# Optimization experiments

Hardware: AMD Instinct MI355X
Metric: run time of the kernel (lower is better)

## Reference

```python
import jax, jax.numpy as jnp
import numpy as np

B, S, T, E, H, VIN, VOUT = 64, 64, 32, 512, 1024, 32000, 32000


def setup_inputs() -> dict:
    key = jax.random.key(0)
    ks = jax.random.split(key, 12)
    rn = lambda k, shape, s=0.02: jax.random.normal(k, shape, jnp.float32) * s
    return {
        "src": jax.random.randint(ks[0], (B, S), 0, VIN),
        "tgt": jax.random.randint(ks[1], (B, T), 0, VOUT),
        "enc_emb": rn(ks[2], (VIN, E)),
        "dec_emb": rn(ks[3], (VOUT, E)),
        "enc_Wih": rn(ks[4], (4 * H, E)),
        "enc_Whh": rn(ks[5], (4 * H, H)),
        "enc_bih": jnp.zeros((4 * H,), jnp.float32),
        "enc_bhh": jnp.zeros((4 * H,), jnp.float32),
        "dec_Wih": rn(ks[6], (4 * H, E + H)),
        "dec_Whh": rn(ks[7], (4 * H, H)),
        "dec_bih": jnp.zeros((4 * H,), jnp.float32),
        "dec_bhh": jnp.zeros((4 * H,), jnp.float32),
        "attn_W": rn(ks[8], (H, 2 * H)),
        "attn_b": jnp.zeros((H,), jnp.float32),
        "v": jax.random.uniform(ks[9], (H,), jnp.float32),
        "fc_W": rn(ks[10], (VOUT, 2 * H)),
        "fc_b": jnp.zeros((VOUT,), jnp.float32),
    }


def _lstm_cell(x, h, c, Wih, Whh, bih, bhh):
    # torch gate order: i, f, g, o
    gates = x @ Wih.T + bih + h @ Whh.T + bhh
    i, f, g, o = jnp.split(gates, 4, axis=-1)
    c_new = jax.nn.sigmoid(f) * c + jax.nn.sigmoid(i) * jnp.tanh(g)
    h_new = jax.nn.sigmoid(o) * jnp.tanh(c_new)
    return h_new, c_new


def _forward(src, tgt, enc_emb, dec_emb, enc_Wih, enc_Whh, enc_bih, enc_bhh,
             dec_Wih, dec_Whh, dec_bih, dec_bhh, attn_W, attn_b, v, fc_W, fc_b):
    b, s = src.shape
    t_len = tgt.shape[1]
    hdim = enc_Whh.shape[1]

    # ---- encoder (single-layer LSTM, batch_first) ----
    x = enc_emb[src]  # [B,S,E] (dropout=0 in eval)

    def enc_step(carry, x_t):
        h, c = carry
        h, c = _lstm_cell(x_t, h, c, enc_Wih, enc_Whh, enc_bih, enc_bhh)
        return (h, c), h

    h0 = jnp.zeros((b, hdim), x.dtype)
    (h_f, c_f), enc_out_tm = jax.lax.scan(enc_step, (h0, h0), jnp.swapaxes(x, 0, 1))
    enc_out = jnp.swapaxes(enc_out_tm, 0, 1)  # [B,S,H]

    # hidden.detach() in torch
    h_f = jax.lax.stop_gradient(h_f)
    c_f = jax.lax.stop_gradient(c_f)

    # split attn_W for the concat(hidden, enc_out) linear
    Wh, We = attn_W[:, :hdim], attn_W[:, hdim:]
    enc_proj = jnp.einsum('bsh,kh->bsk', enc_out, We)  # hoisted, [B,S,H]

    def dec_step(carry, tok):
        h, c = carry
        emb = dec_emb[tok]  # [B,E]
        # Bahdanau attention: tanh(Linear(cat(h, enc_out))) . v
        energy = jnp.tanh(h @ Wh.T[None] if False else jnp.tanh((h @ Wh.T)[:, None, :] + enc_proj + attn_b))
        energy = jnp.tanh((h @ Wh.T)[:, None, :] + enc_proj + attn_b)  # [B,S,H]
        scores = jnp.einsum('bsh,h->bs', energy, v)
        a = jax.nn.softmax(scores, axis=1)
        context = jnp.einsum('bs,bsh->bh', a, enc_out)  # [B,H]
        rnn_in = jnp.concatenate([emb, context], axis=-1)
        h_new, c_new = _lstm_cell(rnn_in, h, c, dec_Wih, dec_Whh, dec_bih, dec_bhh)
        logits = jnp.concatenate([h_new, context], axis=-1) @ fc_W.T + fc_b
        return (h_new, c_new), logits

    # teacher_forcing_ratio = 1.0 -> input at step t is tgt[:, t-1]
    toks_tm = jnp.swapaxes(tgt[:, : t_len - 1], 0, 1)  # [T-1, B]
    _, logits_tm = jax.lax.scan(dec_step, (h_f, c_f), toks_tm)  # [T-1,B,V]
    logits = jnp.swapaxes(logits_tm, 0, 1)  # [B,T-1,V]
    zeros0 = jnp.zeros((b, 1, fc_W.shape[0]), logits.dtype)
    return jnp.concatenate([zeros0, logits], axis=1)  # [B,T,V]


def reference(src, tgt, enc_emb, dec_emb, enc_Wih, enc_Whh, enc_bih, enc_bhh,
              dec_Wih, dec_Whh, dec_bih, dec_bhh, attn_W, attn_b, v, fc_W, fc_b):
    return _forward(src, tgt, enc_emb, dec_emb, enc_Wih, enc_Whh, enc_bih, enc_bhh,
                    dec_Wih, dec_Whh, dec_bih, dec_bhh, attn_W, attn_b, v, fc_W, fc_b)
```

## Files before the change

### kernel.cpp

```cpp
#include <hip/hip_runtime.h>
#include <hip/hip_bf16.h>

typedef __bf16 bf16x8 __attribute__((ext_vector_type(8)));
typedef float  f32x4  __attribute__((ext_vector_type(4)));
typedef _Float16 h16x8 __attribute__((ext_vector_type(8)));

__device__ __forceinline__ unsigned short f2b(float f) {
    union { float f; unsigned u; } w; w.f = f;
    unsigned u = w.u + 0x7FFF + ((w.u >> 16) & 1);
    return (unsigned short)(u >> 16);
}
__device__ __forceinline__ float tanhfast(float x) {
    float e = __expf(2.0f * x);
    return 1.0f - 2.0f / (e + 1.0f);
}

__device__ __forceinline__ void stU(unsigned* p, unsigned v) {
    __hip_atomic_store(p, v, __ATOMIC_RELAXED, __HIP_MEMORY_SCOPE_AGENT);
}
__device__ __forceinline__ void stF(float* p, float v) {
    __hip_atomic_store(p, v, __ATOMIC_RELAXED, __HIP_MEMORY_SCOPE_AGENT);
}
__device__ __forceinline__ int ldI(const int* p) {
    return __hip_atomic_load((int*)p, __ATOMIC_RELAXED, __HIP_MEMORY_SCOPE_AGENT);
}
__device__ __forceinline__ void stI(int* p, int v) {
    __hip_atomic_store(p, v, __ATOMIC_RELAXED, __HIP_MEMORY_SCOPE_AGENT);
}

#define GLD16(g, l) __builtin_amdgcn_global_load_lds( \
    (const __attribute__((address_space(1))) void*)(g), \
    (__attribute__((address_space(3))) void*)(l), 16, 0, 0)

#define SLOT_STRIDE 16
#define NPOLL 256

__device__ __forceinline__ void gbar(int* slots, int* gen, int target) {
    asm volatile("s_waitcnt vmcnt(0)" ::: "memory");
    __syncthreads();
    if (blockIdx.x == 0) {
        if (threadIdx.x == 0) stI(slots, target);
        if (threadIdx.x < NPOLL) {
            while (ldI(slots + threadIdx.x * SLOT_STRIDE) < target)
                __builtin_amdgcn_s_sleep(1);
        }
        __syncthreads();
        if (threadIdx.x == 0) stI(gen, target);
    } else {
        if (threadIdx.x == 0) {
            stI(slots + blockIdx.x * SLOT_STRIDE, target);
            while (ldI(gen) < target)
                __builtin_amdgcn_s_sleep(1);
        }
        __syncthreads();
    }
}

__device__ __forceinline__ void mac8(const unsigned short* A, const unsigned short* B,
                                     f32x4& acc) {
    bf16x8 a[8], b[8];
#pragma unroll
    for (int kk = 0; kk < 8; ++kk) {
        a[kk] = *(const bf16x8*)(A + kk * 32);
        b[kk] = *(const bf16x8*)(B + kk * 32);
    }
#pragma unroll
    for (int kk = 0; kk < 8; ++kk)
        acc = __builtin_amdgcn_mfma_f32_16x16x32_bf16(a[kk], b[kk], acc, 0, 0, 0);
}
__device__ __forceinline__ void mac4(const unsigned short* A, const unsigned short* B,
                                     f32x4& acc) {
    bf16x8 a[4], b[4];
#pragma unroll
    for (int kk = 0; kk < 4; ++kk) {
        a[kk] = *(const bf16x8*)(A + kk * 32);
        b[kk] = *(const bf16x8*)(B + kk * 32);
    }
#pragma unroll
    for (int kk = 0; kk < 4; ++kk)
        acc = __builtin_amdgcn_mfma_f32_16x16x32_bf16(a[kk], b[kk], acc, 0, 0, 0);
}


__global__ void k_gather(const float* __restrict__ emb, const int* __restrict__ tok,
                         unsigned short* __restrict__ out, int L, int ldtok) {
    long total = (long)L * 64 * 128;
    for (long i = (long)blockIdx.x * blockDim.x + threadIdx.x; i < total;
         i += (long)gridDim.x * blockDim.x) {
        int  e4 = (int)(i & 127);
        long r  = i >> 7;
        int  t  = (int)(r >> 6), b = (int)(r & 63);
        int  tk = tok[b * ldtok + t];
        float4 v = *(const float4*)(emb + (long)tk * 512 + e4 * 4);
        ushort4 o; o.x = f2b(v.x); o.y = f2b(v.y); o.z = f2b(v.z); o.w = f2b(v.w);
        *(ushort4*)(out + r * 512 + e4 * 4) = o;
    }
}

__global__ void k_conv(const float* __restrict__ in, unsigned short* __restrict__ out,
                       long N_, int K_, int ldin, int col0, int ldout, int outcol0, int reorder) {
    long total = N_ * (K_ >> 2);
    int kq = K_ >> 2;
    for (long i = (long)blockIdx.x * blockDim.x + threadIdx.x; i < total;
         i += (long)gridDim.x * blockDim.x) {
        long n = i / kq;
        int  k4 = (int)(i - n * kq) * 4;
        long row = reorder ? (long)((n & 3) * 1024 + (n >> 2)) : n;
        float4 v = *(const float4*)(in + row * ldin + col0 + k4);
        ushort4 o; o.x = f2b(v.x); o.y = f2b(v.y); o.z = f2b(v.z); o.w = f2b(v.w);
        *(ushort4*)(out + n * ldout + outcol0 + k4) = o;
    }
}

__global__ void k_bias(const float* __restrict__ b1, const float* __restrict__ b2,
                       float* __restrict__ out) {
    int n = blockIdx.x * blockDim.x + threadIdx.x;
    if (n < 4096) {
        int row = (n & 3) * 1024 + (n >> 2);
        out[n] = b1[row] + b2[row];
    }
}

__global__ void k_zero0(float* __restrict__ out) {
    long total = 64L * 8000;
    for (long i = (long)blockIdx.x * blockDim.x + threadIdx.x; i < total;
         i += (long)gridDim.x * blockDim.x) {
        int b = (int)(i / 8000), q = (int)(i % 8000);
        float4 z = {0.f, 0.f, 0.f, 0.f};
        *(float4*)(out + (long)b * 1024000 + q * 4) = z;
    }
}

template<int BM, int BN, int WGM, int WGN, int FM, int FN>
__device__ __forceinline__ void gemm_core(
    const unsigned short* __restrict__ A, int lda,
    const unsigned short* __restrict__ B, int ldb,
    long m0, long n0, int K,
    unsigned short* As, unsigned short* Bs,
    f32x4 (&acc)[FM][FN])
{
    const int tid  = threadIdx.x;
    const int lane = tid & 63;
    const int wave = tid >> 6;
    const int wm = wave / WGN;
    const int wn = wave % WGN;
    const int srow = lane >> 2;
    const int scol = (lane & 3) * 8;
    const int frow = lane & 15;
    const int fcol = (lane >> 4) * 8;

    for (int k0 = 0; k0 < K; k0 += 32) {
        __syncthreads();
        for (int c = wave; c < BM / 16; c += 4) {
            const unsigned short* g = A + (m0 + c * 16 + srow) * (long)lda + k0 + scol;
            GLD16(g, As + c * 512);
        }
        for (int c = wave; c < BN / 16; c += 4) {
            const unsigned short* g = B + (n0 + c * 16 + srow) * (long)ldb + k0 + scol;
            GLD16(g, Bs + c * 512);
        }
        __syncthreads();
        bf16x8 af[FM], bfr[FN];
#pragma unroll
        for (int m = 0; m < FM; ++m)
            af[m] = *(const bf16x8*)(As + ((wm * FM + m) * 16 + frow) * 32 + fcol);
#pragma unroll
        for (int n = 0; n < FN; ++n)
            bfr[n] = *(const bf16x8*)(Bs + ((wn * FN + n) * 16 + frow) * 32 + fcol);
#pragma unroll
        for (int m = 0; m < FM; ++m)
#pragma unroll
            for (int n = 0; n < FN; ++n)
                acc[m][n] = __builtin_amdgcn_mfma_f32_16x16x32_bf16(af[m], bfr[n], acc[m][n], 0, 0, 0);
    }
}

template<int BM, int BN, int WGM, int WGN, int FM, int FN, int MODE>
__global__ __launch_bounds__(256) void k_gemm(
    const unsigned short* __restrict__ A, int lda,
    const unsigned short* __restrict__ B, int ldb,
    float* __restrict__ C, long ldc, const float* __restrict__ bias,
    int M, int N, int K, int Mreal)
{
    __shared__ __align__(16) unsigned short As[BM * 32];
    __shared__ __align__(16) unsigned short Bs[BN * 32];
    long m0, n0;
    if (MODE == 1) {
        int bid = blockIdx.x;
        int n = (bid & 7) * 32 + (bid >> 7);
        int m = (bid >> 3) & 15;
        if (n >= 250) return;
        m0 = (long)m * BM; n0 = (long)n * BN;
    } else {
        m0 = (long)blockIdx.y * BM; n0 = (long)blockIdx.x * BN;
    }
    f32x4 acc[FM][FN] = {};
    gemm_core<BM, BN, WGM, WGN, FM, FN>(A, lda, B, ldb, m0, n0, K, As, Bs, acc);

    const int lane = threadIdx.x & 63;
    const int wave = threadIdx.x >> 6;
    const int wm = wave / WGN, wn = wave % WGN;
#pragma unroll
    for (int n = 0; n < FN; ++n) {
        long col = n0 + wn * FN * 16 + n * 16 + (lane & 15);
        float bv = bias ? bias[col] : 0.0f;
#pragma unroll
        for (int m = 0; m < FM; ++m) {
            int rl = wm * FM * 16 + m * 16 + (lane >> 4) * 4;
#pragma unroll
            for (int q = 0; q < 4; ++q) {
                long r = m0 + rl + q;
                float val = acc[m][n][q] + bv;
                if (MODE == 0) {
                    C[r * ldc + col] = val;
                } else if (MODE == 2) {
                    ((_Float16*)C)[r * ldc + col] = (_Float16)val;
                } else {
                    if (r < Mreal) {
                        long orow = (r & 63) * 32 + (r >> 6) + 1;
                        C[orow * ldc + col] = val;
                    }
                }
            }
        }
    }
}

__global__ __launch_bounds__(512, 2) void k_enc(
    const unsigned short* __restrict__ W,
    const float* __restrict__ pre,
    unsigned short* __restrict__ hsl,
    unsigned short* __restrict__ enc_out,
    unsigned short* __restrict__ eoT,
    unsigned short* __restrict__ hS0,
    float* __restrict__ cspill,
    int* slots, int* gen)
{
    __shared__ float gs[64 * 16];
    const int blk = blockIdx.x, tid = threadIdx.x;
    const int lane = tid & 63, wave = tid >> 6;
    const int rt = wave >> 1, kh = wave & 1;
    const int n0 = blk * 16;
    const int arow = rt * 16 + (lane & 15);
    const int kch = kh * 512 + (lane >> 4) * 8;
    const int grow = (rt * 16 + (lane >> 4) * 4) * 16 + (lane & 15);
    const unsigned short* Bw = W + (long)(n0 + (lane & 15)) * 1024 + kch;
    const int pb = tid >> 1, pjl = (tid & 1) * 2;
    const int jg = blk * 4 + pjl;
    float c0 = 0.f, c1 = 0.f;
    float4 pr0 = {}, pr1 = {};
    if (tid < 128) {
        pr0 = *(const float4*)(pre + (long)pb * 4096 + n0 + pjl * 4);
        pr1 = *(const float4*)(pre + (long)pb * 4096 + n0 + pjl * 4 + 4);
    }
    int bt = 0;
    for (int t = 0; t < 64; ++t) {
        const unsigned short* Ar = hsl + (long)t * 65536 + (long)arow * 1024 + kch;
        f32x4 acc = {};
        mac8(Ar, Bw, acc);
        mac8(Ar + 256, Bw + 256, acc);
        if (kh == 0) {
#pragma unroll
            for (int q = 0; q < 4; ++q) gs[grow + q * 16] = acc[q];
        }
        __syncthreads();
        if (kh == 1) {
#pragma unroll
            for (int q = 0; q < 4; ++q) atomicAdd(&gs[grow + q * 16], acc[q]);
        }
        __syncthreads();
        if (tid < 128) {
            float4 gA = *(const float4*)(gs + pb * 16 + pjl * 4);
            float4 gB = *(const float4*)(gs + pb * 16 + pjl * 4 + 4);
            float h0v, h1v;
            {
                float gi = gA.x + pr0.x, gf = gA.y + pr0.y, gg = gA.z + pr0.z, go = gA.w + pr0.w;
                float i_ = 1.f / (1.f + __expf(-gi)), f_ = 1.f / (1.f + __expf(-gf));
                float g_ = tanhfast(gg), o_ = 1.f / (1.f + __expf(-go));
                c0 = f_ * c0 + i_ * g_; h0v = o_ * tanhfast(c0);
            }
            {
                float gi = gB.x + pr1.x, gf = gB.y + pr1.y, gg = gB.z + pr1.z, go = gB.w + pr1.w;
                float i_ = 1.f / (1.f + __expf(-gi)), f_ = 1.f / (1.f + __expf(-gf));
                float g_ = tanhfast(gg), o_ = 1.f / (1.f + __expf(-go));
                c1 = f_ * c1 + i_ * g_; h1v = o_ * tanhfast(c1);
            }
            unsigned short hb0 = f2b(h0v), hb1 = f2b(h1v);
            unsigned pk = (unsigned)hb0 | ((unsigned)hb1 << 16);
            stU((unsigned*)(hsl + (long)(t + 1) * 65536 + (long)pb * 1024 + jg), pk);
            *(unsigned*)(enc_out + ((long)pb * 64 + t) * 1024 + jg) = pk;
            eoT[((long)pb * 1024 + jg) * 64 + t]     = hb0;
            eoT[((long)pb * 1024 + jg + 1) * 64 + t] = hb1;
            if (t < 63) {
                pr0 = *(const float4*)(pre + (long)(t + 1) * 262144 + (long)pb * 4096 + n0 + pjl * 4);
                pr1 = *(const float4*)(pre + (long)(t + 1) * 262144 + (long)pb * 4096 + n0 + pjl * 4 + 4);
            } else {
                *(unsigned*)(hS0 + (long)pb * 1024 + jg) = pk;
                cspill[(long)pb * 1024 + jg]     = c0;
                cspill[(long)pb * 1024 + jg + 1] = c1;
            }
        }
        gbar(slots, gen, ++bt);
    }
}

__global__ __launch_bounds__(512, 2) void k_dec(
    const unsigned short* __restrict__ Wh,
    const unsigned short* __restrict__ Wc,
    const float* __restrict__ pre,
    const _Float16* __restrict__ proj16,
    const unsigned short* __restrict__ eoT,
    const float* __restrict__ v,
    const float* __restrict__ cspill,
    unsigned short* __restrict__ hS,
    unsigned short* __restrict__ ctxS,
    float* __restrict__ qS,
    unsigned short* __restrict__ fcin,
    int* slots, int* gen)
{
    __shared__ float gs[64 * 16];
    __shared__ float qv[1024], vv[1024];
    __shared__ float sc[64], al[64];
    const int blk = blockIdx.x, tid = threadIdx.x;
    const int lane = tid & 63, wave = tid >> 6;
    const int rt = wave >> 1, kh = wave & 1;
    const int n0 = blk * 16;
    const int grow = (rt * 16 + (lane >> 4) * 4) * 16 + (lane & 15);
    const int pb = tid >> 1, pjl = (tid & 1) * 2;
    const int jg = blk * 4 + pjl;
    if (tid < 256) {
        float4 v4 = *(const float4*)(v + tid * 4);
        *(float4*)(vv + tid * 4) = v4;
    }
    float c0 = 0.f, c1 = 0.f;
    if (tid < 128) {
        c0 = cspill[(long)pb * 1024 + jg];
        c1 = cspill[(long)pb * 1024 + jg + 1];
    }
    __syncthreads();
    int bt = 0;
    for (int t = 0; t < 31; ++t) {
        const unsigned short* hSt   = hS   + (long)t * 65536;
        const unsigned short* ctxSt = ctxS + (long)t * 65536;
        float4 pr0 = {}, pr1 = {};
        if (tid < 128) {
            pr0 = *(const float4*)(pre + (long)t * 262144 + (long)pb * 4096 + n0 + pjl * 4);
            pr1 = *(const float4*)(pre + (long)t * 262144 + (long)pb * 4096 + n0 + pjl * 4 + 4);
        }
        {
            int nq = blk >> 2, mt = blk & 3;
            if (tid < 256) gs[tid] = 0.f;
            __syncthreads();
            const unsigned short* Ar = hSt + (long)(mt * 16 + (lane & 15)) * 1024
                                           + wave * 128 + (lane >> 4) * 8;
            const unsigned short* Bq = Wh + (long)(nq * 16 + (lane & 15)) * 1024
                                          + wave * 128 + (lane >> 4) * 8;
            f32x4 qa = {};
            mac4(Ar, Bq, qa);
#pragma unroll
            for (int q = 0; q < 4; ++q)
                atomicAdd(&gs[((lane >> 4) * 4 + q) * 16 + (lane & 15)], qa[q]);
            __syncthreads();
            if (tid < 256)
                stF(qS + (long)t * 65536 + (long)(mt * 16 + (tid >> 4)) * 1024
                        + nq * 16 + (tid & 15), gs[tid]);
        }
        gbar(slots, gen, ++bt);
        if (blk < 64) {
            const int b = blk;
            if (tid < 256)
                *(float4*)(qv + tid * 4) =
                    *(const float4*)(qS + (long)t * 65536 + (long)b * 1024 + tid * 4);
            __syncthreads();
            int s = tid >> 3, part = tid & 7;
            const h16x8* pp = (const h16x8*)(proj16 + ((long)b * 64 + s) * 1024 + part * 128);
            float a_ = 0.f;
#pragma unroll 4
            for (int d = 0; d < 16; ++d) {
                h16x8 pv = pp[d];
                int h = part * 128 + d * 8;
#pragma unroll
                for (int j = 0; j < 8; ++j)
                    a_ += vv[h + j] * tanhfast(qv[h + j] + (float)pv[j]);
            }
            a_ += __shfl_xor(a_, 1);
            a_ += __shfl_xor(a_, 2);
            a_ += __shfl_xor(a_, 4);
            if (part == 0) sc[s] = a_;
            __syncthreads();
            if (tid < 64) {
                float x = sc[tid], mx = x;
                for (int o = 32; o; o >>= 1) mx = fmaxf(mx, __shfl_xor(mx, o));
                float e = __expf(x - mx), su = e;
                for (int o = 32; o; o >>= 1) su += __shfl_xor(su, o);
                al[tid] = e / su;
            }
            __syncthreads();
            int h0 = tid * 2;
            float cacc[2];
#pragma unroll
            for (int r = 0; r < 2; ++r) {
                const bf16x8* ep = (const bf16x8*)(eoT + ((long)b * 1024 + h0 + r) * 64);
                float s_ = 0.f;
#pragma unroll
                for (int c8 = 0; c8 < 8; ++c8) {
                    bf16x8 v8 = ep[c8];
#pragma unroll
                    for (int jj = 0; jj < 8; ++jj)
                        s_ += al[c8 * 8 + jj] * (float)v8[jj];
                }
                cacc[r] = s_;
            }
            unsigned pk0 = (unsigned)f2b(cacc[0]) | ((unsigned)f2b(cacc[1]) << 16);
            stU((unsigned*)(ctxS + (long)t * 65536 + (long)b * 1024 + h0), pk0);
            *(unsigned*)(fcin + ((long)t * 64 + b) * 2048 + 1024 + h0) = pk0;
        }
        gbar(slots, gen, ++bt);
        {
            const unsigned short* Asrc = (kh ? ctxSt : hSt)
                + (long)(rt * 16 + (lane & 15)) * 1024 + (lane >> 4) * 8;
            const unsigned short* Bw = Wc + (long)(n0 + (lane & 15)) * 2048
                                          + kh * 1024 + (lane >> 4) * 8;
            f32x4 acc = {};
            mac8(Asrc,       Bw,       acc);
            mac8(Asrc + 256, Bw + 256, acc);
            mac8(Asrc + 512, Bw + 512, acc);
            mac8(Asrc + 768, Bw + 768, acc);
            if (kh == 0) {
#pragma unroll
                for (int q = 0; q < 4; ++q) gs[grow + q * 16] = acc[q];
            }
            __syncthreads();
            if (kh == 1) {
#pragma unroll
                for (int q = 0; q < 4; ++q) atomicAdd(&gs[grow + q * 16], acc[q]);
            }
            __syncthreads();
            if (tid < 128) {
                float4 gA = *(const float4*)(gs + pb * 16 + pjl * 4);
                float4 gB = *(const float4*)(gs + pb * 16 + pjl * 4 + 4);
                float h0v, h1v;
                {
                    float gi = gA.x + pr0.x, gf = gA.y + pr0.y, gg = gA.z + pr0.z, go = gA.w + pr0.w;
                    float i_ = 1.f / (1.f + __expf(-gi)), f_ = 1.f / (1.f + __expf(-gf));
                    float g_ = tanhfast(gg), o_ = 1.f / (1.f + __expf(-go));
                    c0 = f_ * c0 + i_ * g_; h0v = o_ * tanhfast(c0);
                }
                {
                    float gi = gB.x + pr1.x, gf = gB.y + pr1.y, gg = gB.z + pr1.z, go = gB.w + pr1.w;
                    float i_ = 1.f / (1.f + __expf(-gi)), f_ = 1.f / (1.f + __expf(-gf));
                    float g_ = tanhfast(gg), o_ = 1.f / (1.f + __expf(-go));
                    c1 = f_ * c1 + i_ * g_; h1v = o_ * tanhfast(c1);
                }
                unsigned pk = (unsigned)f2b(h0v) | ((unsigned)f2b(h1v) << 16);
                stU((unsigned*)(hS + (long)(t + 1) * 65536 + (long)pb * 1024 + jg), pk);
                *(unsigned*)(fcin + ((long)t * 64 + pb) * 2048 + jg) = pk;
            }
        }
        gbar(slots, gen, ++bt);
    }
}

extern "C" void kernel_launch(void* const* d_in, const int* in_sizes, int n_in,
                              void* d_out, int out_size, void* d_ws, size_t ws_size,
                              hipStream_t stream) {
    const int*   src     = (const int*)d_in[0];
    const int*   tgt     = (const int*)d_in[1];
    const float* enc_emb = (const float*)d_in[2];
    const float* dec_emb = (const float*)d_in[3];
    const float* enc_Wih = (const float*)d_in[4];
    const float* enc_Whh = (const float*)d_in[5];
    const float* enc_bih = (const float*)d_in[6];
    const float* enc_bhh = (const float*)d_in[7];
    const float* dec_Wih = (const float*)d_in[8];
    const float* dec_Whh = (const float*)d_in[9];
    const float* dec_bih = (const float*)d_in[10];
    const float* dec_bhh = (const float*)d_in[11];
    const float* attn_W  = (const float*)d_in[12];
    const float* attn_b  = (const float*)d_in[13];
    const float* vvec    = (const float*)d_in[14];
    const float* fc_W    = (const float*)d_in[15];
    const float* fc_b    = (const float*)d_in[16];
    float* out = (float*)d_out;

    char* ws = (char*)d_ws;
    size_t off = 0;
    auto alloc = [&](size_t bytes) -> char* {
        off = (off + 255) & ~(size_t)255;
        char* p = ws + off; off += bytes; return p;
    };
    unsigned short* wX      = (unsigned short*)alloc(4096UL * 512 * 2);
    unsigned short* weWih   = (unsigned short*)alloc(4096UL * 512 * 2);
    unsigned short* weWhh   = (unsigned short*)alloc(4096UL * 1024 * 2);
    float*          ebias   = (float*)alloc(4096UL * 4);
    float*          pre_enc = (float*)alloc(4096UL * 4096 * 4);
    unsigned short* enc_out = (unsigned short*)alloc(4096UL * 1024 * 2);
    unsigned short* eoT     = (unsigned short*)alloc(64UL * 1024 * 64 * 2);
    unsigned short* wWe     = (unsigned short*)alloc(1024UL * 1024 * 2);
    unsigned short* wWh     = (unsigned short*)alloc(1024UL * 1024 * 2);
    _Float16*       proj16  = (_Float16*)alloc(4096UL * 1024 * 2);
    float*          cbuf    = (float*)alloc(64UL * 1024 * 4);
    unsigned short* demb    = (unsigned short*)alloc(2048UL * 512 * 2);
    unsigned short* wDemb   = (unsigned short*)alloc(4096UL * 512 * 2);
    unsigned short* wCat    = (unsigned short*)alloc(4096UL * 2048 * 2);
    float*          dbias   = (float*)alloc(4096UL * 4);
    float*          pre_dec = (float*)alloc(2048UL * 4096 * 4);
    unsigned short* fcin    = (unsigned short*)alloc(2048UL * 2048 * 2);
    unsigned short* wFc     = (unsigned short*)alloc(32000UL * 2048 * 2);
    unsigned short* hslE    = (unsigned short*)alloc(65UL * 65536 * 2);
    unsigned short* hS      = (unsigned short*)alloc(32UL * 65536 * 2);
    unsigned short* ctxS    = (unsigned short*)alloc(32UL * 65536 * 2);
    float*          qS      = (float*)alloc(32UL * 65536 * 4);
    int*            bar     = (int*)alloc(65536);
    (void)ws_size; (void)in_sizes; (void)n_in; (void)out_size;

    int* slotsE = bar;
    int* genE   = bar + 4096;
    int* slotsD = bar + 8192;
    int* genD   = bar + 12288;

    hipMemsetAsync(bar, 0, 65536, stream);
    hipMemsetAsync(hslE, 0, 65536UL * 2, stream);
    k_zero0<<<512, 256, 0, stream>>>(out);

    k_gather<<<2048, 256, 0, stream>>>(enc_emb, src, wX, 64, 64);
    k_gather<<<1024, 256, 0, stream>>>(dec_emb, tgt, demb, 31, 32);
    k_conv<<<2048, 256, 0, stream>>>(enc_Wih, weWih, 4096, 512, 512, 0, 512, 0, 1);
    k_conv<<<2048, 256, 0, stream>>>(enc_Whh, weWhh, 4096, 1024, 1024, 0, 1024, 0, 1);
    k_conv<<<2048, 256, 0, stream>>>(dec_Wih, wDemb, 4096, 512, 1536, 0, 512, 0, 1);
    k_conv<<<2048, 256, 0, stream>>>(dec_Whh, wCat, 4096, 1024, 1024, 0, 2048, 0, 1);
    k_conv<<<2048, 256, 0, stream>>>(dec_Wih, wCat, 4096, 1024, 1536, 512, 2048, 1024, 1);
    k_conv<<<2048, 256, 0, stream>>>(attn_W, wWh, 1024, 1024, 2048, 0, 1024, 0, 0);
    k_conv<<<2048, 256, 0, stream>>>(attn_W, wWe, 1024, 1024, 2048, 1024, 1024, 0, 0);
    k_conv<<<4096, 256, 0, stream>>>(fc_W, wFc, 32000, 2048, 2048, 0, 2048, 0, 0);
    k_bias<<<16, 256, 0, stream>>>(enc_bih, enc_bhh, ebias);
    k_bias<<<16, 256, 0, stream>>>(dec_bih, dec_bhh, dbias);

    k_gemm<128,128,2,2,4,4,0><<<dim3(32, 32), 256, 0, stream>>>(
        wX, 512, weWih, 512, pre_enc, 4096, ebias, 4096, 4096, 512, 4096);
    k_gemm<128,128,2,2,4,4,0><<<dim3(32, 16), 256, 0, stream>>>(
        demb, 512, wDemb, 512, pre_dec, 4096, dbias, 2048, 4096, 512, 2048);

    k_enc<<<256, 512, 0, stream>>>(weWhh, pre_enc, hslE, enc_out, eoT,
                                   hS, cbuf, slotsE, genE);

    k_gemm<128,128,2,2,4,4,2><<<dim3(8, 32), 256, 0, stream>>>(
        enc_out, 1024, wWe, 1024, (float*)proj16, 1024, attn_b, 4096, 1024, 1024, 4096);

    k_dec<<<256, 512, 0, stream>>>(wWh, wCat, pre_dec, proj16, eoT, vvec, cbuf,
                                   hS, ctxS, qS, fcin, slotsD, genD);

    k_gemm<128,128,2,2,4,4,1><<<dim3(4096), 256, 0, stream>>>(
        fcin, 2048, wFc, 2048, out, 32000, fc_b, 2048, 32000, 2048, 1984);
}
```

Before: 2.595 ms.

## Keep recurrent weights resident in LDS with 128 persistent 1024-thread blocks

The persistent encoder and decoder kernels now run 128 blocks of 1024 threads instead of 256 blocks of 512, and each block owns 32 gate columns. At kernel start each block loads its slice of the recurrent weight matrix into LDS (64 KB for the encoder, 128 KB for the decoder), so every time step reads the MFMA B operands from LDS instead of global memory. The decoder also splits the hidden and context halves of its gate GEMM so the hidden half runs before the attention barrier, overlapping it with the query projection. This lowers per-step global traffic and barrier participants, at the cost of half as many blocks, large LDS use, more shared atomics, and 16-bit atomic stores for h.

New measurement: 3.121 ms. 20.3% more time.

```diff
diff --git a/kernel.cpp b/kernel.cpp
--- a/kernel.cpp
+++ b/kernel.cpp
@@ -18,6 +18,9 @@
 __device__ __forceinline__ void stU(unsigned* p, unsigned v) {
     __hip_atomic_store(p, v, __ATOMIC_RELAXED, __HIP_MEMORY_SCOPE_AGENT);
 }
+__device__ __forceinline__ void stS(unsigned short* p, unsigned short v) {
+    __hip_atomic_store(p, v, __ATOMIC_RELAXED, __HIP_MEMORY_SCOPE_AGENT);
+}
 __device__ __forceinline__ void stF(float* p, float v) {
     __hip_atomic_store(p, v, __ATOMIC_RELAXED, __HIP_MEMORY_SCOPE_AGENT);
 }
@@ -33,14 +36,13 @@
     (__attribute__((address_space(3))) void*)(l), 16, 0, 0)
 
 #define SLOT_STRIDE 16
-#define NPOLL 256
-
-__device__ __forceinline__ void gbar(int* slots, int* gen, int target) {
+
+__device__ __forceinline__ void gbar(int* slots, int* gen, int target, int nblk) {
     asm volatile("s_waitcnt vmcnt(0)" ::: "memory");
     __syncthreads();
     if (blockIdx.x == 0) {
         if (threadIdx.x == 0) stI(slots, target);
-        if (threadIdx.x < NPOLL) {
+        if ((int)threadIdx.x < nblk) {
             while (ldI(slots + threadIdx.x * SLOT_STRIDE) < target)
                 __builtin_amdgcn_s_sleep(1);
         }
@@ -56,17 +58,15 @@
     }
 }
 
-__device__ __forceinline__ void mac8(const unsigned short* A, const unsigned short* B,
-                                     f32x4& acc) {
-    bf16x8 a[8], b[8];
-#pragma unroll
-    for (int kk = 0; kk < 8; ++kk) {
-        a[kk] = *(const bf16x8*)(A + kk * 32);
-        b[kk] = *(const bf16x8*)(B + kk * 32);
-    }
+template<int STR>
+__device__ __forceinline__ void mac8L(const unsigned short* A, const bf16x8* BL,
+                                      f32x4& acc) {
+    bf16x8 a[8];
+#pragma unroll
+    for (int kk = 0; kk < 8; ++kk) a[kk] = *(const bf16x8*)(A + kk * 32);
 #pragma unroll
     for (int kk = 0; kk < 8; ++kk)
-        acc = __builtin_amdgcn_mfma_f32_16x16x32_bf16(a[kk], b[kk], acc, 0, 0, 0);
+        acc = __builtin_amdgcn_mfma_f32_16x16x32_bf16(a[kk], BL[kk * STR], acc, 0, 0, 0);
 }
 __device__ __forceinline__ void mac4(const unsigned short* A, const unsigned short* B,
                                      f32x4& acc) {
@@ -226,7 +226,7 @@
     }
 }
 
-__global__ __launch_bounds__(512, 2) void k_enc(
+__global__ __launch_bounds__(1024, 1) void k_enc(
     const unsigned short* __restrict__ W,
     const float* __restrict__ pre,
     unsigned short* __restrict__ hsl,
@@ -236,75 +236,59 @@
     float* __restrict__ cspill,
     int* slots, int* gen)
 {
-    __shared__ float gs[64 * 16];
+    __shared__ __align__(16) unsigned short WL[32 * 1024];
+    __shared__ float gs[64 * 32];
     const int blk = blockIdx.x, tid = threadIdx.x;
     const int lane = tid & 63, wave = tid >> 6;
-    const int rt = wave >> 1, kh = wave & 1;
-    const int n0 = blk * 16;
-    const int arow = rt * 16 + (lane & 15);
-    const int kch = kh * 512 + (lane >> 4) * 8;
-    const int grow = (rt * 16 + (lane >> 4) * 4) * 16 + (lane & 15);
-    const unsigned short* Bw = W + (long)(n0 + (lane & 15)) * 1024 + kch;
-    const int pb = tid >> 1, pjl = (tid & 1) * 2;
-    const int jg = blk * 4 + pjl;
-    float c0 = 0.f, c1 = 0.f;
-    float4 pr0 = {}, pr1 = {};
-    if (tid < 128) {
-        pr0 = *(const float4*)(pre + (long)pb * 4096 + n0 + pjl * 4);
-        pr1 = *(const float4*)(pre + (long)pb * 4096 + n0 + pjl * 4 + 4);
-    }
+    const int cg = wave >> 3, rt = (wave >> 1) & 3, kh = wave & 1;
+    const int n0 = blk * 32;
+    const int pb = tid >> 3, pj = tid & 7;
+    const int jg = blk * 8 + pj;
+    for (int i = tid; i < 4096; i += 1024) {
+        int r = i & 31, k8 = i >> 5;
+        ((bf16x8*)WL)[k8 * 32 + r] = *(const bf16x8*)(W + (long)(n0 + r) * 1024 + k8 * 8);
+    }
+    const bf16x8* BL = (const bf16x8*)WL + ((long)(kh * 64 + (lane >> 4))) * 32 + cg * 16 + (lane & 15);
+    const int arowoff = (rt * 16 + (lane & 15)) * 1024 + kh * 512 + (lane >> 4) * 8;
+    const int grow = (rt * 16 + (lane >> 4) * 4) * 32 + cg * 16 + (lane & 15);
+    float c0 = 0.f;
+    float4 pr = {};
+    if (tid < 512) pr = *(const float4*)(pre + (long)pb * 4096 + n0 + pj * 4);
+    __syncthreads();
     int bt = 0;
     for (int t = 0; t < 64; ++t) {
-        const unsigned short* Ar = hsl + (long)t * 65536 + (long)arow * 1024 + kch;
+        gs[tid] = 0.f; gs[tid + 1024] = 0.f;
+        __syncthreads();
+        const unsigned short* Ar = hsl + (long)t * 65536 + arowoff;
         f32x4 acc = {};
-        mac8(Ar, Bw, acc);
-        mac8(Ar + 256, Bw + 256, acc);
-        if (kh == 0) {
-#pragma unroll
-            for (int q = 0; q < 4; ++q) gs[grow + q * 16] = acc[q];
-        }
+        mac8L<128>(Ar,       BL,        acc);
+        mac8L<128>(Ar + 256, BL + 1024, acc);
+#pragma unroll
+        for (int q = 0; q < 4; ++q) atomicAdd(&gs[grow + q * 32], acc[q]);
         __syncthreads();
-        if (kh == 1) {
-#pragma unroll
-            for (int q = 0; q < 4; ++q) atomicAdd(&gs[grow + q * 16], acc[q]);
-        }
-        __syncthreads();
-        if (tid < 128) {
-            float4 gA = *(const float4*)(gs + pb * 16 + pjl * 4);
-            float4 gB = *(const float4*)(gs + pb * 16 + pjl * 4 + 4);
-            float h0v, h1v;
-            {
-                float gi = gA.x + pr0.x, gf = gA.y + pr0.y, gg = gA.z + pr0.z, go = gA.w + pr0.w;
-                float i_ = 1.f / (1.f + __expf(-gi)), f_ = 1.f / (1.f + __expf(-gf));
-                float g_ = tanhfast(gg), o_ = 1.f / (1.f + __expf(-go));
-                c0 = f_ * c0 + i_ * g_; h0v = o_ * tanhfast(c0);
-            }
-            {
-                float gi = gB.x + pr1.x, gf = gB.y + pr1.y, gg = gB.z + pr1.z, go = gB.w + pr1.w;
-                float i_ = 1.f / (1.f + __expf(-gi)), f_ = 1.f / (1.f + __expf(-gf));
-                float g_ = tanhfast(gg), o_ = 1.f / (1.f + __expf(-go));
-                c1 = f_ * c1 + i_ * g_; h1v = o_ * tanhfast(c1);
-            }
-            unsigned short hb0 = f2b(h0v), hb1 = f2b(h1v);
-            unsigned pk = (unsigned)hb0 | ((unsigned)hb1 << 16);
-            stU((unsigned*)(hsl + (long)(t + 1) * 65536 + (long)pb * 1024 + jg), pk);
-            *(unsigned*)(enc_out + ((long)pb * 64 + t) * 1024 + jg) = pk;
-            eoT[((long)pb * 1024 + jg) * 64 + t]     = hb0;
-            eoT[((long)pb * 1024 + jg + 1) * 64 + t] = hb1;
+        if (tid < 512) {
+            float4 g4 = *(const float4*)(gs + pb * 32 + pj * 4);
+            float gi = g4.x + pr.x, gf = g4.y + pr.y, gg = g4.z + pr.z, go = g4.w + pr.w;
+            float i_ = 1.f / (1.f + __expf(-gi)), f_ = 1.f / (1.f + __expf(-gf));
+            float g_ = tanhfast(gg), o_ = 1.f / (1.f + __expf(-go));
+            c0 = f_ * c0 + i_ * g_;
+            float hv = o_ * tanhfast(c0);
+            unsigned short hb = f2b(hv);
+            stS(hsl + (long)(t + 1) * 65536 + (long)pb * 1024 + jg, hb);
+            enc_out[((long)pb * 64 + t) * 1024 + jg] = hb;
+            eoT[((long)pb * 1024 + jg) * 64 + t] = hb;
             if (t < 63) {
-                pr0 = *(const float4*)(pre + (long)(t + 1) * 262144 + (long)pb * 4096 + n0 + pjl * 4);
-                pr1 = *(const float4*)(pre + (long)(t + 1) * 262144 + (long)pb * 4096 + n0 + pjl * 4 + 4);
+                pr = *(const float4*)(pre + (long)(t + 1) * 262144 + (long)pb * 4096 + n0 + pj * 4);
             } else {
-                *(unsigned*)(hS0 + (long)pb * 1024 + jg) = pk;
-                cspill[(long)pb * 1024 + jg]     = c0;
-                cspill[(long)pb * 1024 + jg + 1] = c1;
-            }
-        }
-        gbar(slots, gen, ++bt);
-    }
-}
-
-__global__ __launch_bounds__(512, 2) void k_dec(
+                stS(hS0 + (long)pb * 1024 + jg, hb);
+                cspill[(long)pb * 1024 + jg] = c0;
+            }
+        }
+        gbar(slots, gen, ++bt, 128);
+    }
+}
+
+__global__ __launch_bounds__(1024, 1) void k_dec(
     const unsigned short* __restrict__ Wh,
     const unsigned short* __restrict__ Wc,
     const float* __restrict__ pre,
@@ -318,67 +302,78 @@
     unsigned short* __restrict__ fcin,
     int* slots, int* gen)
 {
-    __shared__ float gs[64 * 16];
+    __shared__ __align__(16) unsigned short WcL[32 * 2048];
+    __shared__ float gs1[32 * 16];
+    __shared__ float gs2[64 * 32];
     __shared__ float qv[1024], vv[1024];
     __shared__ float sc[64], al[64];
     const int blk = blockIdx.x, tid = threadIdx.x;
     const int lane = tid & 63, wave = tid >> 6;
-    const int rt = wave >> 1, kh = wave & 1;
-    const int n0 = blk * 16;
-    const int grow = (rt * 16 + (lane >> 4) * 4) * 16 + (lane & 15);
-    const int pb = tid >> 1, pjl = (tid & 1) * 2;
-    const int jg = blk * 4 + pjl;
-    if (tid < 256) {
-        float4 v4 = *(const float4*)(v + tid * 4);
-        *(float4*)(vv + tid * 4) = v4;
-    }
-    float c0 = 0.f, c1 = 0.f;
-    if (tid < 128) {
-        c0 = cspill[(long)pb * 1024 + jg];
-        c1 = cspill[(long)pb * 1024 + jg + 1];
-    }
+    const int n0 = blk * 32;
+    const int cg = wave >> 3, rt = (wave >> 1) & 3, kh = wave & 1;
+    const int rs = wave >> 3, kq = wave & 7;
+    const int nq = blk >> 1, mt = blk & 1;
+    const int pb = tid >> 3, pj = tid & 7;
+    const int jg = blk * 8 + pj;
+    for (int i = tid; i < 8192; i += 1024) {
+        int r = i & 31, k8 = i >> 5;
+        ((bf16x8*)WcL)[k8 * 32 + r] = *(const bf16x8*)(Wc + (long)(n0 + r) * 2048 + k8 * 8);
+    }
+    const bf16x8* BLh = (const bf16x8*)WcL + ((long)(kh * 64 + (lane >> 4))) * 32 + cg * 16 + (lane & 15);
+    const bf16x8* BLc = BLh + 128L * 32;
+    const int garow = (rt * 16 + (lane & 15)) * 1024 + kh * 512 + (lane >> 4) * 8;
+    const int grow = (rt * 16 + (lane >> 4) * 4) * 32 + cg * 16 + (lane & 15);
+    vv[tid] = v[tid];
+    float c0 = 0.f;
+    if (tid < 512) c0 = cspill[(long)pb * 1024 + jg];
     __syncthreads();
     int bt = 0;
     for (int t = 0; t < 31; ++t) {
         const unsigned short* hSt   = hS   + (long)t * 65536;
         const unsigned short* ctxSt = ctxS + (long)t * 65536;
-        float4 pr0 = {}, pr1 = {};
-        if (tid < 128) {
-            pr0 = *(const float4*)(pre + (long)t * 262144 + (long)pb * 4096 + n0 + pjl * 4);
-            pr1 = *(const float4*)(pre + (long)t * 262144 + (long)pb * 4096 + n0 + pjl * 4 + 4);
-        }
+        float4 pr = {};
+        if (tid < 512)
+            pr = *(const float4*)(pre + (long)t * 262144 + (long)pb * 4096 + n0 + pj * 4);
         {
-            int nq = blk >> 2, mt = blk & 3;
-            if (tid < 256) gs[tid] = 0.f;
+            if (tid < 512) gs1[tid] = 0.f;
+            gs2[tid] = 0.f; gs2[tid + 1024] = 0.f;
             __syncthreads();
-            const unsigned short* Ar = hSt + (long)(mt * 16 + (lane & 15)) * 1024
-                                           + wave * 128 + (lane >> 4) * 8;
-            const unsigned short* Bq = Wh + (long)(nq * 16 + (lane & 15)) * 1024
-                                          + wave * 128 + (lane >> 4) * 8;
-            f32x4 qa = {};
-            mac4(Ar, Bq, qa);
-#pragma unroll
-            for (int q = 0; q < 4; ++q)
-                atomicAdd(&gs[((lane >> 4) * 4 + q) * 16 + (lane & 15)], qa[q]);
+            {
+                const unsigned short* Ar = hSt + (long)(mt * 32 + rs * 16 + (lane & 15)) * 1024
+                                               + kq * 128 + (lane >> 4) * 8;
+                const unsigned short* Bq = Wh + (long)(nq * 16 + (lane & 15)) * 1024
+                                              + kq * 128 + (lane >> 4) * 8;
+                f32x4 qa = {};
+                mac4(Ar, Bq, qa);
+#pragma unroll
+                for (int q = 0; q < 4; ++q)
+                    atomicAdd(&gs1[(rs * 16 + (lane >> 4) * 4 + q) * 16 + (lane & 15)], qa[q]);
+            }
+            {
+                const unsigned short* Ah = hSt + garow;
+                f32x4 acc = {};
+                mac8L<128>(Ah,       BLh,        acc);
+                mac8L<128>(Ah + 256, BLh + 1024, acc);
+#pragma unroll
+                for (int q = 0; q < 4; ++q) atomicAdd(&gs2[grow + q * 32], acc[q]);
+            }
             __syncthreads();
-            if (tid < 256)
-                stF(qS + (long)t * 65536 + (long)(mt * 16 + (tid >> 4)) * 1024
-                        + nq * 16 + (tid & 15), gs[tid]);
-        }
-        gbar(slots, gen, ++bt);
+            if (tid < 512)
+                stF(qS + (long)t * 65536 + (long)(mt * 32 + (tid >> 4)) * 1024
+                        + nq * 16 + (tid & 15), gs1[tid]);
+        }
+        gbar(slots, gen, ++bt, 128);
         if (blk < 64) {
             const int b = blk;
-            if (tid < 256)
-                *(float4*)(qv + tid * 4) =
-                    *(const float4*)(qS + (long)t * 65536 + (long)b * 1024 + tid * 4);
+            qv[tid] = qS[(long)t * 65536 + (long)b * 1024 + tid];
             __syncthreads();
-            int s = tid >> 3, part = tid & 7;
-            const h16x8* pp = (const h16x8*)(proj16 + ((long)b * 64 + s) * 1024 + part * 128);
+            int s = tid >> 4, part = tid & 15;
+            const h16x8* pp = (const h16x8*)(proj16 + ((long)b * 64 + s) * 1024 + part * 64);
             float a_ = 0.f;
-#pragma unroll 4
-            for (int d = 0; d < 16; ++d) {
+#pragma unroll
+            for (int d = 0; d < 8; ++d) {
                 h16x8 pv = pp[d];
-                int h = part * 128 + d * 8;
+                int h = part * 64 + d * 8;
 #pragma unroll
                 for (int j = 0; j < 8; ++j)
                     a_ += vv[h + j] * tanhfast(qv[h + j] + (float)pv[j]);
@@ -386,6 +381,7 @@
             a_ += __shfl_xor(a_, 1);
             a_ += __shfl_xor(a_, 2);
             a_ += __shfl_xor(a_, 4);
+            a_ += __shfl_xor(a_, 8);
             if (part == 0) sc[s] = a_;
             __syncthreads();
             if (tid < 64) {
@@ -396,68 +392,49 @@
                 al[tid] = e / su;
             }
             __syncthreads();
-            int h0 = tid * 2;
-            float cacc[2];
-#pragma unroll
-            for (int r = 0; r < 2; ++r) {
-                const bf16x8* ep = (const bf16x8*)(eoT + ((long)b * 1024 + h0 + r) * 64);
-                float s_ = 0.f;
-#pragma unroll
-                for (int c8 = 0; c8 < 8; ++c8) {
-                    bf16x8 v8 = ep[c8];
-#pragma unroll
-                    for (int jj = 0; jj < 8; ++jj)
-                        s_ += al[c8 * 8 + jj] * (float)v8[jj];
+            if (tid < 512) {
+                int h0 = tid * 2;
+                float cacc[2];
+#pragma unroll
+                for (int r = 0; r < 2; ++r) {
+                    const bf16x8* ep = (const bf16x8*)(eoT + ((long)b * 1024 + h0 + r) * 64);
+                    float s_ = 0.f;
+#pragma unroll
+                    for (int c8 = 0; c8 < 8; ++c8) {
+                        bf16x8 v8 = ep[c8];
+#pragma unroll
+                        for (int jj = 0; jj < 8; ++jj)
+                            s_ += al[c8 * 8 + jj] * (float)v8[jj];
+                    }
+                    cacc[r] = s_;
                 }
-                cacc[r] = s_;
-            }
-            unsigned pk0 = (unsigned)f2b(cacc[0]) | ((unsigned)f2b(cacc[1]) << 16);
-            stU((unsigned*)(ctxS + (long)t * 65536 + (long)b * 1024 + h0), pk0);
-            *(unsigned*)(fcin + ((long)t * 64 + b) * 2048 + 1024 + h0) = pk0;
-        }
-        gbar(slots, gen, ++bt);
+                unsigned pk0 = (unsigned)f2b(cacc[0]) | ((unsigned)f2b(cacc[1]) << 16);
+                stU((unsigned*)(ctxS + (long)t * 65536 + (long)b * 1024 + h0), pk0);
+                *(unsigned*)(fcin + ((long)t * 64 + b) * 2048 + 1024 + h0) = pk0;
+            }
+        }
+        gbar(slots, gen, ++bt, 128);
         {
-            const unsigned short* Asrc = (kh ? ctxSt : hSt)
-                + (long)(rt * 16 + (lane & 15)) * 1024 + (lane >> 4) * 8;
-            const unsigned short* Bw = Wc + (long)(n0 + (lane & 15)) * 2048
-                                          + kh * 1024 + (lane >> 4) * 8;
+            const unsigned short* Ac = ctxSt + garow;
             f32x4 acc = {};
-            mac8(Asrc,       Bw,       acc);
-            mac8(Asrc + 256, Bw + 256, acc);
-            mac8(Asrc + 512, Bw + 512, acc);
-            mac8(Asrc + 768, Bw + 768, acc);
-            if (kh == 0) {
-#pragma unroll
-                for (int q = 0; q < 4; ++q) gs[grow + q * 16] = acc[q];
-            }
+            mac8L<128>(Ac,       BLc,        acc);
+            mac8L<128>(Ac + 256, BLc + 1024, acc);
+#pragma unroll
+            for (int q = 0; q < 4; ++q) atomicAdd(&gs2[grow + q * 32], acc[q]);
             __syncthreads();
-            if (kh == 1) {
-#pragma unroll
-                for (int q = 0; q < 4; ++q) atomicAdd(&gs[grow + q * 16], acc[q]);
-            }
-            __syncthreads();
-            if (tid < 128) {
-                float4 gA = *(const float4*)(gs + pb * 16 + pjl * 4);
-                float4 gB = *(const float4*)(gs + pb * 16 + pjl * 4 + 4);
-                float h0v, h1v;
-                {
-                    float gi = gA.x + pr0.x, gf = gA.y + pr0.y, gg = gA.z + pr0.z, go = gA.w + pr0.w;
-                    float i_ = 1.f / (1.f + __expf(-gi)), f_ = 1.f / (1.f + __expf(-gf));
-                    float g_ = tanhfast(gg), o_ = 1.f / (1.f + __expf(-go));
-                    c0 = f_ * c0 + i_ * g_; h0v = o_ * tanhfast(c0);
-                }
-                {
-                    float gi = gB.x + pr1.x, gf = gB.y + pr1.y, gg = gB.z + pr1.z, go = gB.w + pr1.w;
-                    float i_ = 1.f / (1.f + __expf(-gi)), f_ = 1.f / (1.f + __expf(-gf));
-                    float g_ = tanhfast(gg), o_ = 1.f / (1.f + __expf(-go));
-                    c1 = f_ * c1 + i_ * g_; h1v = o_ * tanhfast(c1);
-                }
-                unsigned pk = (unsigned)f2b(h0v) | ((unsigned)f2b(h1v) << 16);
-                stU((unsigned*)(hS + (long)(t + 1) * 65536 + (long)pb * 1024 + jg), pk);
-                *(unsigned*)(fcin + ((long)t * 64 + pb) * 2048 + jg) = pk;
-            }
-        }
-        gbar(slots, gen, ++bt);
+            if (tid < 512) {
+                float4 g4 = *(const float4*)(gs2 + pb * 32 + pj * 4);
+                float gi = g4.x + pr.x, gf = g4.y + pr.y, gg = g4.z + pr.z, go = g4.w + pr.w;
+                float i_ = 1.f / (1.f + __expf(-gi)), f_ = 1.f / (1.f + __expf(-gf));
+                float g_ = tanhfast(gg), o_ = 1.f / (1.f + __expf(-go));
+                c0 = f_ * c0 + i_ * g_;
+                float hv = o_ * tanhfast(c0);
+                unsigned short hb = f2b(hv);
+                stS(hS + (long)(t + 1) * 65536 + (long)pb * 1024 + jg, hb);
+                fcin[((long)t * 64 + pb) * 2048 + jg] = hb;
+            }
+        }
+        gbar(slots, gen, ++bt, 128);
     }
 }
 
@@ -541,14 +518,14 @@
     k_gemm<128,128,2,2,4,4,0><<<dim3(32, 16), 256, 0, stream>>>(
         demb, 512, wDemb, 512, pre_dec, 4096, dbias, 2048, 4096, 512, 2048);
 
-    k_enc<<<256, 512, 0, stream>>>(weWhh, pre_enc, hslE, enc_out, eoT,
-                                   hS, cbuf, slotsE, genE);
+    k_enc<<<128, 1024, 0, stream>>>(weWhh, pre_enc, hslE, enc_out, eoT,
+                                    hS, cbuf, slotsE, genE);
 
     k_gemm<128,128,2,2,4,4,2><<<dim3(8, 32), 256, 0, stream>>>(
         enc_out, 1024, wWe, 1024, (float*)proj16, 1024, attn_b, 4096, 1024, 1024, 4096);
 
-    k_dec<<<256, 512, 0, stream>>>(wWh, wCat, pre_dec, proj16, eoT, vvec, cbuf,
-                                   hS, ctxS, qS, fcin, slotsD, genD);
+    k_dec<<<128, 1024, 0, stream>>>(wWh, wCat, pre_dec, proj16, eoT, vvec, cbuf,
+                                    hS, ctxS, qS, fcin, slotsD, genD);
 
     k_gemm<128,128,2,2,4,4,1><<<dim3(4096), 256, 0, stream>>>(
         fcin, 2048, wFc, 2048, out, 32000, fc_b, 2048, 32000, 2048, 1984);
```
